# Performance work log

Measured on AMD Instinct MI355X. Metric: run time of the kernel, lower is better.

The kernel has to match this reference:

```python
import jax, jax.numpy as jnp
import numpy as np
import math

# init config (matches init_kwargs); sigma/alpha are squared in __init__
SIGMA2 = 8.0 ** 2
ALPHA2 = 8.0 ** 2
C_SIZE = 512
STRIDE = 8
MINX = 1e-06
M = 100                      # ratio=100 > 1 -> M = int(ratio), capped at 100
K = C_SIZE // STRIDE         # 64 grid cells per axis
G = K * K                    # 4096 density-field cells
B, N = 8, 512                # images, annotated points per image
TWO_PI = 2.0 * math.pi


def setup_inputs():
    key = jax.random.key(0)
    k1, _ = jax.random.split(key)
    points = jax.random.uniform(k1, (B, N, 2), dtype=jnp.float32) * C_SIZE
    st_sizes = jnp.full((B,), float(C_SIZE), dtype=jnp.float32)
    return {"points": points, "st_sizes": st_sizes}


def _per_image(pts, cood):
    # pts: [N,2]; cood: [K]
    x = pts[:, 0]
    y = pts[:, 1]
    dx = x[:, None] - cood[None, :]                 # [N,K]
    dy = y[:, None] - cood[None, :]                 # [N,K]
    # dis_all = y_dis[:, :, None] + x_dis[:, None, :] flattened: g = iy*K + ix
    dis = (dy[:, :, None] ** 2 + dx[:, None, :] ** 2).reshape(pts.shape[0], G)  # [N,G]
    s1 = ALPHA2 + SIGMA2
    s2 = ALPHA2 + SIGMA2 / 2.0
    m = jnp.exp(-0.5 / s1 * dis) / (TWO_PI * s1)    # [N,G]
    tv = jnp.exp(-0.5 / s2 * dis) / (TWO_PI * s2)
    v = (tv / (TWO_PI * 2.0 * SIGMA2)).sum(0) - (m ** 2).sum(0)   # [G] (sel_v == v, no bg)
    # top-M cells by sel_v, then sort indices ascending (ratio>1 branch -> static M)
    inds = jnp.argsort(-v)
    Minds = jnp.sort(inds[:M])                      # [M]
    v = jnp.maximum(v, MINX)                        # add=False -> clamp
    # xf[n, iy*K+ix] = x_n - cood[ix]; yf[n, iy*K+ix] = y_n - cood[iy]
    iy = Minds // K
    ix = Minds % K
    xfM = dx[:, ix]                                 # [N,M]
    yfM = dy[:, iy]                                 # [N,M]
    df = (xfM[:, None, :] - xfM[:, :, None]) ** 2 + (yfM[:, None, :] - yfM[:, :, None]) ** 2
    af = (0.5 * (xfM[:, None, :] + xfM[:, :, None])) ** 2 + (0.5 * (yfM[:, None, :] + yfM[:, :, None])) ** 2
    g1 = jnp.exp(-0.5 / (2.0 * SIGMA2) * df) / (TWO_PI * 2.0 * SIGMA2)          # [N,M,M]
    tmpv2 = (g1 * (jnp.exp(-0.5 / s2 * af) / (TWO_PI * s2))).sum(0) + g1.sum(0)  # [M,M]
    disM = dis[:, Minds]                            # [N,M]
    tmpm2 = jnp.exp(-0.5 / s1 * disM) / (TWO_PI * s1)
    A = tmpv2 - tmpm2.T @ tmpm2                     # [M,M]
    eye = jnp.eye(M, dtype=bool)
    A = jnp.where(eye, 1e-10, A)                    # diag overwritten to 1e-10
    vM = v[Minds] + 1e-10
    tmpA = vM[:, None] * jnp.linalg.inv(A) * vM[None, :] + jnp.diag(vM)
    Bm = jnp.linalg.inv(tmpA)
    return m, v, A, Bm, Minds


def reference(points, st_sizes):
    # st_sizes only matters for use_background=True; kept for signature fidelity
    cood = jnp.arange(0, C_SIZE, STRIDE, dtype=jnp.float32) + STRIDE / 2.0
    m, v, A, Bm, Minds = jax.vmap(lambda p: _per_image(p, cood))(points)
    return m, v, A, Bm, Minds
```

## Files before the change

kernel.cpp:

```cpp
#include <hip/hip_runtime.h>
#include <math.h>

#ifndef M_PI
#define M_PI 3.14159265358979323846
#endif

#define BB 8
#define NN 512
#define KK 64
#define GG 4096
#define MM 100

#define SZ_VD    (BB*GG*8u*2u)
#define OFF_VD   0u
#define SZ_VM    (BB*MM*4u)
#define OFF_VM   (OFF_VD + SZ_VD)
#define SZ_AD    (BB*MM*MM*4u)
#define OFF_AD   (OFF_VM + SZ_VM)

#define OUT_M  0
#define OUT_V  (BB*NN*GG)
#define OUT_A  (OUT_V + BB*GG)
#define OUT_B  (OUT_A + BB*MM*MM)
#define OUT_MI (OUT_B + BB*MM*MM)

#define MU_PER 8
#define MU_VP 4096
#define MU_AS 2048
#define MU_IV 10240

__device__ __forceinline__ void m_units(const float* __restrict__ pts,
                                        float* __restrict__ out, int u0, int cnt) {
  const float CM = (float)(1.0/(2.0*M_PI*128.0));
  for (int k = 0; k < cnt; ++k) {
    int u = u0 + k;
    int t = u*256 + (int)threadIdx.x;
    int e = t << 2;
    int img = e >> 21;
    int rem = e & ((1 << 21) - 1);
    int n = rem >> 12;
    int g = rem & 4095;
    int iy = g >> 6, ix = g & 63;
    float x = pts[(img*NN + n)*2 + 0];
    float y = pts[(img*NN + n)*2 + 1];
    float dy = y - (8.0f*iy + 4.0f);
    float ey = __expf(dy*dy*(-0.5f/128.0f));
    float4 r;
    float dx0 = x - (8.0f*ix + 4.0f);
    float dx1 = x - (8.0f*(ix+1) + 4.0f);
    float dx2 = x - (8.0f*(ix+2) + 4.0f);
    float dx3 = x - (8.0f*(ix+3) + 4.0f);
    r.x = ey*__expf(dx0*dx0*(-0.5f/128.0f))*CM;
    r.y = ey*__expf(dx1*dx1*(-0.5f/128.0f))*CM;
    r.z = ey*__expf(dx2*dx2*(-0.5f/128.0f))*CM;
    r.w = ey*__expf(dx3*dx3*(-0.5f/128.0f))*CM;
    *reinterpret_cast<float4*>(&out[OUT_M + e]) = r;
  }
}

__device__ __forceinline__ void m_units512(const float* __restrict__ pts,
                                           float* __restrict__ out, int u0, int cnt) {
  const float CM = (float)(1.0/(2.0*M_PI*128.0));
  for (int k = 0; k < cnt/2; ++k) {
    int t = u0*256 + k*512 + (int)threadIdx.x;
    int e = t << 2;
    int img = e >> 21;
    int rem = e & ((1 << 21) - 1);
    int n = rem >> 12;
    int g = rem & 4095;
    int iy = g >> 6, ix = g & 63;
    float x = pts[(img*NN + n)*2 + 0];
    float y = pts[(img*NN + n)*2 + 1];
    float dy = y - (8.0f*iy + 4.0f);
    float ey = __expf(dy*dy*(-0.5f/128.0f));
    float4 r;
    float dx0 = x - (8.0f*ix + 4.0f);
    float dx1 = x - (8.0f*(ix+1) + 4.0f);
    float dx2 = x - (8.0f*(ix+2) + 4.0f);
    float dx3 = x - (8.0f*(ix+3) + 4.0f);
    r.x = ey*__expf(dx0*dx0*(-0.5f/128.0f))*CM;
    r.y = ey*__expf(dx1*dx1*(-0.5f/128.0f))*CM;
    r.z = ey*__expf(dx2*dx2*(-0.5f/128.0f))*CM;
    r.w = ey*__expf(dx3*dx3*(-0.5f/128.0f))*CM;
    *reinterpret_cast<float4*>(&out[OUT_M + e]) = r;
  }
}

__device__ __forceinline__ float flt_readlane(float v, int l) {
  return __int_as_float(__builtin_amdgcn_readlane(__float_as_int(v), l));
}

__global__ __launch_bounds__(256) void k_vpart(const float* __restrict__ pts,
                                               double* __restrict__ vd,
                                               float* __restrict__ out) {
  __shared__ double sEy2[16][66], sEy3[16][66], sEx2[16][66], sEx3[16][66];
  __shared__ float px[256], py[256];
  int bid = blockIdx.x;
  if (bid >= BB*32) { m_units(pts, out, (bid - BB*32)*MU_PER, MU_PER); return; }
  int half = bid & 1;
  int rem = bid >> 1;
  int tile = rem & 15;
  int img = rem >> 4;
  int iy0 = (tile >> 2) << 4;
  int ix0 = (tile & 3) << 4;
  int tx = threadIdx.x & 15, ty = threadIdx.x >> 4;
  int n = threadIdx.x & 63;
  int tbl = threadIdx.x >> 6;
  for (int s = threadIdx.x; s < 256; s += 256) {
    px[s] = pts[(img*NN + half*256 + s)*2 + 0];
    py[s] = pts[(img*NN + half*256 + s)*2 + 1];
  }
  const double alpha = (tbl & 1) ? (1.0/128.0) : (0.5/96.0);
  const double Q = exp(-128.0*alpha);
  const int base = (tbl >= 2) ? ix0 : iy0;
  double* dst = (tbl == 0) ? &sEy2[0][0] : (tbl == 1) ? &sEy3[0][0]
              : (tbl == 2) ? &sEx2[0][0] : &sEx3[0][0];
  double aV = 0.0, aM = 0.0;
  for (int kc = 0; kc < 4; ++kc) {
    int nbl = kc << 6;
    __syncthreads();
    {
      int nn = nbl + n;
      double coord = (tbl >= 2) ? (double)px[nn] : (double)py[nn];
      double d0 = coord - (8.0*base + 4.0);
      double E = exp(-alpha*d0*d0);
      double R = exp(alpha*(16.0*d0 - 64.0));
      #pragma unroll
      for (int row = 0; row < 16; ++row) {
        dst[row*66 + n] = E;
        E *= R; R *= Q;
      }
    }
    __syncthreads();
    #pragma unroll 8
    for (int n2 = 0; n2 < 64; ++n2) {
      aV += sEy2[ty][n2]*sEx2[tx][n2];
      aM += sEy3[ty][n2]*sEx3[tx][n2];
    }
  }
  const double CTV = 1.0/((2.0*M_PI*96.0)*(2.0*M_PI*128.0));
  const double CM2 = 1.0/((2.0*M_PI*128.0)*(2.0*M_PI*128.0));
  vd[half*(BB*GG) + img*GG + (iy0 + ty)*KK + ix0 + tx] = CTV*aV - CM2*aM;
}

union AselU {
  struct {
    unsigned int ku[GG];
    unsigned int hist4[4][256];
    unsigned int wq[4];
    unsigned int sPref, sMask;
    unsigned int sRem, sPickB, sPickRem, sCGt, sCEq;
    int tie[128];
  } se;
  struct {
    float sxi[16][130], syi[16][130], sti[16][130];
    float sxj[16][130], syj[16][130], stj[16][130];
    float px[NN], py[NN];
    float cxi[16], cyi[16], cxj[16], cyj[16];
  } ka;
};

__device__ __forceinline__ void bitonic128(int* a, int tid) {
  for (int kk = 2; kk <= 128; kk <<= 1)
    for (int jj = kk >> 1; jj > 0; jj >>= 1) {
      if (tid < 128) {
        int p = tid ^ jj;
        if (p > tid) {
          int x = a[tid], y = a[p];
          bool up = ((tid & kk) == 0);
          if (up ? (x > y) : (x < y)) { a[tid] = y; a[p] = x; }
        }
      }
      __syncthreads();
    }
}

__global__ __launch_bounds__(256) void k_Asel(const float* __restrict__ pts,
                                              const double* __restrict__ vd,
                                              float* __restrict__ out,
                                              float* __restrict__ ad,
                                              float* __restrict__ vm) {
  __shared__ AselU u;
  __shared__ int selFinal[128];
  int bid = blockIdx.x;
  if (bid >= BB*28) { m_units(pts, out, MU_VP + (bid - BB*28)*MU_PER, MU_PER); return; }
  int img = bid / 28;
  int tile = bid - img*28;
  bool tile0 = (tile == 0);
  int tid = threadIdx.x;
  int wv = tid >> 6;
  int lane = tid & 63;

  for (int t = 0; t < 16; ++t) {
    int g = t*256 + tid;
    float v = (float)(vd[img*GG + g] + vd[BB*GG + img*GG + g]);
    if (tile0) out[OUT_V + img*GG + g] = fmaxf(v, 1e-6f);
    int w = __float_as_int(v);
    u.se.ku[g] = (w < 0) ? ~(unsigned)w : ((unsigned)w | 0x80000000u);
  }
  if (tid == 0) {
    u.se.sRem = 100; u.se.sPref = 0u; u.se.sMask = 0u;
    u.se.sCGt = 0; u.se.sCEq = 0;
  }
  for (int shift = 24; shift >= 0; shift -= 8) {
    for (int c = 0; c < 4; ++c) u.se.hist4[c][tid] = 0;
    __syncthreads();
    unsigned mask = u.se.sMask, pref = u.se.sPref;
    for (int t = 0; t < 16; ++t) {
      unsigned k = u.se.ku[t*256 + tid];
      if ((k & mask) == pref)
        atomicAdd(&u.se.hist4[wv][(k >> shift) & 255u], 1u);
    }
    __syncthreads();
    unsigned tot = u.se.hist4[0][tid] + u.se.hist4[1][tid]
                 + u.se.hist4[2][tid] + u.se.hist4[3][tid];
    unsigned val = tot;
    #pragma unroll
    for (int off = 1; off < 64; off <<= 1) {
      unsigned o = (unsigned)__shfl_down((int)val, off);
      if (lane + off < 64) val += o;
    }
    if (lane == 0) u.se.wq[wv] = val;
    __syncthreads();
    unsigned suf = val;
    for (int w2 = wv + 1; w2 < 4; ++w2) suf += u.se.wq[w2];
    unsigned rem = u.se.sRem;
    unsigned sgt = suf - tot;
    if (suf >= rem && sgt < rem) { u.se.sPickB = (unsigned)tid; u.se.sPickRem = rem - sgt; }
    __syncthreads();
    if (tid == 0) {
      u.se.sPref |= u.se.sPickB << shift;
      u.se.sMask |= 255u << shift;
      u.se.sRem   = u.se.sPickRem;
    }
    __syncthreads();
  }
  unsigned T = u.se.sPref;
  for (int t = 0; t < 16; ++t) {
    int g = t*256 + tid;
    unsigned k = u.se.ku[g];
    if (k > T) {
      unsigned p = atomicAdd(&u.se.sCGt, 1u);
      selFinal[p] = g;
    } else if (k == T) {
      unsigned p = atomicAdd(&u.se.sCEq, 1u);
      if (p < 128) u.se.tie[p] = g;
    }
  }
  __syncthreads();
  unsigned cgt = u.se.sCGt, ceq = u.se.sCEq, r = u.se.sRem;
  if (tid < 128 && tid >= (int)((ceq < 128u) ? ceq : 128u)) u.se.tie[tid] = 0x7fffffff;
  __syncthreads();
  bitonic128(u.se.tie, tid);
  if (tid < (int)r) selFinal[cgt + tid] = u.se.tie[tid];
  if (tid >= MM && tid < 128) selFinal[tid] = 0x7fffffff;
  __syncthreads();
  bitonic128(selFinal, tid);
  if (tile0 && tid < MM) {
    int mi = selFinal[tid];
    out[OUT_MI + img*MM + tid] = (float)mi;
    float vsel = (float)(vd[img*GG + mi] + vd[BB*GG + img*GG + mi]);
    vm[img*MM + tid] = fmaxf(vsel, 1e-6f) + 1e-10f;
  }
  __syncthreads();

  int it = 0, trem = tile;
  while (trem >= 7 - it) { trem -= 7 - it; ++it; }
  int jt = it + trem;
  int i0 = it*16, j0 = jt*16;
  int tj = tid & 15, ti = tid >> 4;
  int i = i0 + ti, j = j0 + tj;
  const float CM = (float)(1.0/(2.0*M_PI*128.0));
  const float C1 = (float)(1.0/(2.0*M_PI*128.0));
  const float C2 = (float)(1.0/(2.0*M_PI*96.0));
  for (int s = tid; s < NN; s += 256) {
    u.ka.px[s] = pts[(img*NN + s)*2 + 0];
    u.ka.py[s] = pts[(img*NN + s)*2 + 1];
  }
  if (tid < 16) {
    int gi = i0 + tid; if (gi > 99) gi = 99;
    int mi = selFinal[gi];
    u.ka.cxi[tid] = 8.0f*(mi & 63) + 4.0f;
    u.ka.cyi[tid] = 8.0f*(mi >> 6) + 4.0f;
  } else if (tid < 32) {
    int rr = tid - 16;
    int gj = j0 + rr; if (gj > 99) gj = 99;
    int mj = selFinal[gj];
    u.ka.cxj[rr] = 8.0f*(mj & 63) + 4.0f;
    u.ka.cyj[rr] = 8.0f*(mj >> 6) + 4.0f;
  }
  float aV = 0.0f, aM = 0.0f;
  for (int nc = 0; nc < NN; nc += 128) {
    __syncthreads();
    for (int s = tid; s < 16*128; s += 256) {
      int row = s >> 7, n = s & 127;
      float x = u.ka.px[nc + n], y = u.ka.py[nc + n];
      float fxi = x - u.ka.cxi[row], fyi = y - u.ka.cyi[row];
      u.ka.sxi[row][n] = fxi; u.ka.syi[row][n] = fyi;
      u.ka.sti[row][n] = __expf((fxi*fxi + fyi*fyi)*(-0.5f/128.0f))*CM;
      float fxj = x - u.ka.cxj[row], fyj = y - u.ka.cyj[row];
      u.ka.sxj[row][n] = fxj; u.ka.syj[row][n] = fyj;
      u.ka.stj[row][n] = __expf((fxj*fxj + fyj*fyj)*(-0.5f/128.0f))*CM;
    }
    __syncthreads();
    #pragma unroll 4
    for (int n = 0; n < 128; ++n) {
      float xi = u.ka.sxi[ti][n], yi = u.ka.syi[ti][n], tii = u.ka.sti[ti][n];
      float xj = u.ka.sxj[tj][n], yj = u.ka.syj[tj][n], tjj = u.ka.stj[tj][n];
      float ddx = xj - xi, ddy = yj - yi;
      float df = ddx*ddx + ddy*ddy;
      float sx = 0.5f*(xi + xj), sy = 0.5f*(yi + yj);
      float af = sx*sx + sy*sy;
      float g1 = __expf(df*(-0.5f/128.0f))*C1;
      float h  = __expf(af*(-0.5f/96.0f))*C2;
      aV += g1 + g1*h;
      aM += tii*tjj;
    }
  }
  if (i < 100 && j < 100) {
    float val = (i == j) ? 1e-10f : (float)((double)aV - (double)aM);
    out[OUT_A + (img*MM + i)*MM + j] = val;
    ad[(img*MM + i)*MM + j] = val;
    if (it != jt) {
      out[OUT_A + (img*MM + j)*MM + i] = val;
      ad[(img*MM + j)*MM + i] = val;
    }
  }
}

#define PRS 130
__global__ __launch_bounds__(512)
void k_inv_m(const float* __restrict__ ad,
             const float* __restrict__ vm,
             const float* __restrict__ pts,
             float* __restrict__ out) {
  __shared__ float S[128*17];
  __shared__ float Pr[16*PRS];
  __shared__ float svm[112];
  if (blockIdx.x >= BB) {
    m_units512(pts, out, MU_VP + MU_AS + ((int)blockIdx.x - BB)*MU_PER, MU_PER);
    return;
  }
  int img = blockIdx.x;
  int tx = threadIdx.x & 31, ty = threadIdx.x >> 5;
  float C[7][4];
  if (threadIdx.x < 100) svm[threadIdx.x] = vm[img*MM + threadIdx.x];
  #pragma unroll
  for (int a = 0; a < 7; ++a) {
    int r = ty + 16*a;
    #pragma unroll
    for (int b = 0; b < 4; ++b) {
      int col = tx + 32*b;
      float v2 = (r < 100 && col < 100) ? ad[(img*MM + r)*MM + col] : 0.0f;
      if (r == col && r < 100) v2 += vm[img*MM + r];
      C[a][b] = v2;
    }
  }
  for (int p = 0; p < 7; ++p) {
    int k0 = p*16;
    int nbp = (p == 6) ? 4 : 16;
    {
      int bp = p >> 1;
      bool mine = ((tx >> 4) == (p & 1));
      int cq = tx & 15;
      #pragma unroll
      for (int a = 0; a < 7; ++a) {
        int r = ty + 16*a;
        if (mine) {
          float val = 0.0f;
          #pragma unroll
          for (int b = 0; b < 4; ++b) if (b == bp) val = C[a][b];
          S[r*17 + cq] = (r < 100 && cq < nbp) ? val : 0.0f;
        }
      }
    }
    {
      float pv[4];
      #pragma unroll
      for (int b = 0; b < 4; ++b) pv[b] = 0.0f;
      #pragma unroll
      for (int a = 0; a < 7; ++a) {
        #pragma unroll
        for (int b = 0; b < 4; ++b) if (a == p) pv[b] = C[a][b];
      }
      #pragma unroll
      for (int b = 0; b < 4; ++b) Pr[ty*PRS + tx + 32*b] = pv[b];
    }
    __syncthreads();
    if (threadIdx.x < 64) {
      int lane = threadIdx.x;
      float P0[16], P1[16];
      #pragma unroll
      for (int c = 0; c < 16; ++c) {
        P0[c] = S[lane*17 + c];
        P1[c] = (lane + 64 < 112) ? S[(lane + 64)*17 + c] : 0.0f;
      }
      #pragma unroll
      for (int kk = 0; kk < 16; ++kk) {
        if (kk < nbp) {
          int kg = k0 + kk;
          int r1 = lane + 64;
          bool khigh = kg >= 64; int kl = kg & 63;
          float pivinv = 1.0f / flt_readlane(khigh ? P1[kk] : P0[kk], kl);
          float pr[16];
          #pragma unroll
          for (int c = 0; c < 16; ++c) {
            float pv = flt_readlane(khigh ? P1[c] : P0[c], kl);
            pr[c] = (c == kk) ? pivinv : pv*pivinv;
          }
          {
            float f = P0[kk];
            if (lane == kg) {
              #pragma unroll
              for (int c = 0; c < 16; ++c) P0[c] = pr[c];
            } else {
              #pragma unroll
              for (int c = 0; c < 16; ++c) P0[c] = ((c == kk) ? 0.0f : P0[c]) - f*pr[c];
            }
          }
          {
            float f = P1[kk];
            if (r1 == kg) {
              #pragma unroll
              for (int c = 0; c < 16; ++c) P1[c] = pr[c];
            } else {
              #pragma unroll
              for (int c = 0; c < 16; ++c) P1[c] = ((c == kk) ? 0.0f : P1[c]) - f*pr[c];
            }
          }
        }
      }
      #pragma unroll
      for (int c = 0; c < 16; ++c) {
        S[lane*17 + c] = P0[c];
        if (lane + 64 < 112) S[(lane + 64)*17 + c] = P1[c];
      }
    }
    __syncthreads();
    #pragma unroll
    for (int a = 0; a < 7; ++a) {
      int r = ty + 16*a;
      bool prow_ = (r >= k0) && (r < k0 + 16);
      #pragma unroll
      for (int b = 0; b < 4; ++b) {
        int col = tx + 32*b;
        if (r >= 100 || (col >> 4) == p || prow_) C[a][b] = 0.0f;
      }
    }
    #pragma unroll 4
    for (int t = 0; t < 16; ++t) {
      bool tok = (t < nbp);
      float bt[4], sa[7];
      #pragma unroll
      for (int b = 0; b < 4; ++b) bt[b] = tok ? Pr[t*PRS + tx + 32*b] : 0.0f;
      #pragma unroll
      for (int a = 0; a < 7; ++a) sa[a] = S[(ty + 16*a)*17 + t];
      #pragma unroll
      for (int a = 0; a < 7; ++a)
        #pragma unroll
        for (int b = 0; b < 4; ++b) C[a][b] += sa[a]*bt[b];
    }
    #pragma unroll
    for (int a = 0; a < 7; ++a) {
      int r = ty + 16*a;
      #pragma unroll
      for (int b = 0; b < 4; ++b) {
        int col = tx + 32*b;
        if ((col >> 4) == p) C[a][b] = S[r*17 + (col & 15)];
      }
    }
    __syncthreads();
  }
  #pragma unroll
  for (int a = 0; a < 7; ++a) {
    int r = ty + 16*a; if (r >= 100) continue;
    float dinv = 1.0f / svm[r];
    #pragma unroll
    for (int b = 0; b < 4; ++b) {
      int col = tx + 32*b; if (col >= 100) continue;
      float val = ((col == r) ? dinv : 0.0f) - C[a][b];
      out[OUT_B + (img*MM + r)*MM + col] = val;
    }
  }
}

extern "C" void kernel_launch(void* const* d_in, const int* in_sizes, int n_in,
                              void* d_out, int out_size, void* d_ws, size_t ws_size,
                              hipStream_t stream) {
  const float* pts = (const float*)d_in[0];
  float* out = (float*)d_out;
  char* ws = (char*)d_ws;
  double* vd  = (double*)(ws + OFF_VD);
  float* vmd = (float*)(ws + OFF_VM);
  float* ad  = (float*)(ws + OFF_AD);

  hipLaunchKernelGGL(k_vpart, dim3(BB*32 + MU_VP/MU_PER), dim3(256), 0, stream, pts, vd, out);
  hipLaunchKernelGGL(k_Asel, dim3(BB*28 + MU_AS/MU_PER), dim3(256), 0, stream, pts, vd, out, ad, vmd);
  hipLaunchKernelGGL(k_inv_m, dim3(BB + MU_IV/MU_PER), dim3(512), 0, stream, ad, vmd, pts, out);
}
```

Baseline: 195.8 us.

## Split v partial sums four ways, spread histogram atomics, wave-level bitonic sort

The v-field reduction kernel now splits the 512 points into four quarters instead of two, doubling the number of blocks, and reads LDS as double2 pairs. The top-M radix select spreads its histogram over 32 padded copies to reduce LDS atomic contention. The two block-wide bitonic sorts with many __syncthreads become a single-wave register sort using shuffles. In exchange, the workspace grows, k_Asel must read four partial buffers, and clearing and summing the histograms costs more.

```diff
diff --git a/kernel.cpp b/kernel.cpp
--- a/kernel.cpp
+++ b/kernel.cpp
@@ -11,7 +11,7 @@
 #define GG 4096
 #define MM 100
 
-#define SZ_VD    (BB*GG*8u*2u)
+#define SZ_VD    (BB*GG*8u*4u)
 #define OFF_VD   0u
 #define SZ_VM    (BB*MM*4u)
 #define OFF_VM   (OFF_VD + SZ_VD)
@@ -94,11 +94,11 @@
                                                double* __restrict__ vd,
                                                float* __restrict__ out) {
   __shared__ double sEy2[16][66], sEy3[16][66], sEx2[16][66], sEx3[16][66];
-  __shared__ float px[256], py[256];
+  __shared__ float px[128], py[128];
   int bid = blockIdx.x;
-  if (bid >= BB*32) { m_units(pts, out, (bid - BB*32)*MU_PER, MU_PER); return; }
-  int half = bid & 1;
-  int rem = bid >> 1;
+  if (bid >= BB*64) { m_units(pts, out, (bid - BB*64)*MU_PER, MU_PER); return; }
+  int quarter = bid & 3;
+  int rem = bid >> 2;
   int tile = rem & 15;
   int img = rem >> 4;
   int iy0 = (tile >> 2) << 4;
@@ -106,9 +106,9 @@
   int tx = threadIdx.x & 15, ty = threadIdx.x >> 4;
   int n = threadIdx.x & 63;
   int tbl = threadIdx.x >> 6;
-  for (int s = threadIdx.x; s < 256; s += 256) {
-    px[s] = pts[(img*NN + half*256 + s)*2 + 0];
-    py[s] = pts[(img*NN + half*256 + s)*2 + 1];
+  if (threadIdx.x < 128) {
+    px[threadIdx.x] = pts[(img*NN + quarter*128 + threadIdx.x)*2 + 0];
+    py[threadIdx.x] = pts[(img*NN + quarter*128 + threadIdx.x)*2 + 1];
   }
   const double alpha = (tbl & 1) ? (1.0/128.0) : (0.5/96.0);
   const double Q = exp(-128.0*alpha);
@@ -116,7 +116,7 @@
   double* dst = (tbl == 0) ? &sEy2[0][0] : (tbl == 1) ? &sEy3[0][0]
               : (tbl == 2) ? &sEx2[0][0] : &sEx3[0][0];
   double aV = 0.0, aM = 0.0;
-  for (int kc = 0; kc < 4; ++kc) {
+  for (int kc = 0; kc < 2; ++kc) {
     int nbl = kc << 6;
     __syncthreads();
     {
@@ -133,20 +133,24 @@
     }
     __syncthreads();
     #pragma unroll 8
-    for (int n2 = 0; n2 < 64; ++n2) {
-      aV += sEy2[ty][n2]*sEx2[tx][n2];
-      aM += sEy3[ty][n2]*sEx3[tx][n2];
+    for (int n2 = 0; n2 < 64; n2 += 2) {
+      double2 y2 = *reinterpret_cast<const double2*>(&sEy2[ty][n2]);
+      double2 x2 = *reinterpret_cast<const double2*>(&sEx2[tx][n2]);
+      double2 y3 = *reinterpret_cast<const double2*>(&sEy3[ty][n2]);
+      double2 x3 = *reinterpret_cast<const double2*>(&sEx3[tx][n2]);
+      aV += y2.x*x2.x; aV += y2.y*x2.y;
+      aM += y3.x*x3.x; aM += y3.y*x3.y;
     }
   }
   const double CTV = 1.0/((2.0*M_PI*96.0)*(2.0*M_PI*128.0));
   const double CM2 = 1.0/((2.0*M_PI*128.0)*(2.0*M_PI*128.0));
-  vd[half*(BB*GG) + img*GG + (iy0 + ty)*KK + ix0 + tx] = CTV*aV - CM2*aM;
+  vd[quarter*(BB*GG) + img*GG + (iy0 + ty)*KK + ix0 + tx] = CTV*aV - CM2*aM;
 }
 
 union AselU {
   struct {
     unsigned int ku[GG];
-    unsigned int hist4[4][256];
+    unsigned int hist[32][257];
     unsigned int wq[4];
     unsigned int sPref, sMask;
     unsigned int sRem, sPickB, sPickRem, sCGt, sCEq;
@@ -160,19 +164,24 @@
   } ka;
 };
 
-__device__ __forceinline__ void bitonic128(int* a, int tid) {
-  for (int kk = 2; kk <= 128; kk <<= 1)
-    for (int jj = kk >> 1; jj > 0; jj >>= 1) {
-      if (tid < 128) {
-        int p = tid ^ jj;
-        if (p > tid) {
-          int x = a[tid], y = a[p];
-          bool up = ((tid & kk) == 0);
-          if (up ? (x > y) : (x < y)) { a[tid] = y; a[p] = x; }
-        }
-      }
-      __syncthreads();
-    }
+__device__ __forceinline__ void wave_sort128(int* a) {
+  int L = (int)(threadIdx.x & 63);
+  int e0 = a[2*L], e1 = a[2*L + 1];
+  for (int kk = 2; kk <= 128; kk <<= 1) {
+    for (int jj = kk >> 1; jj >= 2; jj >>= 1) {
+      int pl = jj >> 1;
+      int o0 = __shfl_xor(e0, pl);
+      int o1 = __shfl_xor(e1, pl);
+      bool upper = (L & pl) != 0;
+      bool up = ((2*L) & kk) == 0;
+      if (up != upper) { e0 = min(e0, o0); e1 = min(e1, o1); }
+      else             { e0 = max(e0, o0); e1 = max(e1, o1); }
+    }
+    bool up = ((2*L) & kk) == 0;
+    int lo = min(e0, e1), hi = max(e0, e1);
+    e0 = up ? lo : hi; e1 = up ? hi : lo;
+  }
+  a[2*L] = e0; a[2*L + 1] = e1;
 }
 
 __global__ __launch_bounds__(256) void k_Asel(const float* __restrict__ pts,
@@ -190,10 +199,12 @@
   int tid = threadIdx.x;
   int wv = tid >> 6;
   int lane = tid & 63;
+  int hc = tid >> 3;
 
   for (int t = 0; t < 16; ++t) {
     int g = t*256 + tid;
-    float v = (float)(vd[img*GG + g] + vd[BB*GG + img*GG + g]);
+    float v = (float)(((vd[img*GG + g] + vd[BB*GG + img*GG + g])
+                     + vd[2*BB*GG + img*GG + g]) + vd[3*BB*GG + img*GG + g]);
     if (tile0) out[OUT_V + img*GG + g] = fmaxf(v, 1e-6f);
     int w = __float_as_int(v);
     u.se.ku[g] = (w < 0) ? ~(unsigned)w : ((unsigned)w | 0x80000000u);
@@ -203,17 +214,18 @@
     u.se.sCGt = 0; u.se.sCEq = 0;
   }
   for (int shift = 24; shift >= 0; shift -= 8) {
-    for (int c = 0; c < 4; ++c) u.se.hist4[c][tid] = 0;
+    for (int s = tid; s < 32*257; s += 256) (&u.se.hist[0][0])[s] = 0;
     __syncthreads();
     unsigned mask = u.se.sMask, pref = u.se.sPref;
     for (int t = 0; t < 16; ++t) {
       unsigned k = u.se.ku[t*256 + tid];
       if ((k & mask) == pref)
-        atomicAdd(&u.se.hist4[wv][(k >> shift) & 255u], 1u);
-    }
-    __syncthreads();
-    unsigned tot = u.se.hist4[0][tid] + u.se.hist4[1][tid]
-                 + u.se.hist4[2][tid] + u.se.hist4[3][tid];
+        atomicAdd(&u.se.hist[hc][(k >> shift) & 255u], 1u);
+    }
+    __syncthreads();
+    unsigned tot = 0;
+    #pragma unroll
+    for (int c = 0; c < 32; ++c) tot += u.se.hist[c][tid];
     unsigned val = tot;
     #pragma unroll
     for (int off = 1; off < 64; off <<= 1) {
@@ -251,15 +263,18 @@
   unsigned cgt = u.se.sCGt, ceq = u.se.sCEq, r = u.se.sRem;
   if (tid < 128 && tid >= (int)((ceq < 128u) ? ceq : 128u)) u.se.tie[tid] = 0x7fffffff;
   __syncthreads();
-  bitonic128(u.se.tie, tid);
+  if (tid < 64) wave_sort128(u.se.tie);
+  __syncthreads();
   if (tid < (int)r) selFinal[cgt + tid] = u.se.tie[tid];
   if (tid >= MM && tid < 128) selFinal[tid] = 0x7fffffff;
   __syncthreads();
-  bitonic128(selFinal, tid);
+  if (tid < 64) wave_sort128(selFinal);
+  __syncthreads();
   if (tile0 && tid < MM) {
     int mi = selFinal[tid];
     out[OUT_MI + img*MM + tid] = (float)mi;
-    float vsel = (float)(vd[img*GG + mi] + vd[BB*GG + img*GG + mi]);
+    float vsel = (float)(((vd[img*GG + mi] + vd[BB*GG + img*GG + mi])
+                        + vd[2*BB*GG + img*GG + mi]) + vd[3*BB*GG + img*GG + mi]);
     vm[img*MM + tid] = fmaxf(vsel, 1e-6f) + 1e-10f;
   }
   __syncthreads();
@@ -494,7 +509,7 @@
   float* vmd = (float*)(ws + OFF_VM);
   float* ad  = (float*)(ws + OFF_AD);
 
-  hipLaunchKernelGGL(k_vpart, dim3(BB*32 + MU_VP/MU_PER), dim3(256), 0, stream, pts, vd, out);
+  hipLaunchKernelGGL(k_vpart, dim3(BB*64 + MU_VP/MU_PER), dim3(256), 0, stream, pts, vd, out);
   hipLaunchKernelGGL(k_Asel, dim3(BB*28 + MU_AS/MU_PER), dim3(256), 0, stream, pts, vd, out, ad, vmd);
   hipLaunchKernelGGL(k_inv_m, dim3(BB + MU_IV/MU_PER), dim3(512), 0, stream, ad, vmd, pts, out);
 }
```

Result: no change. 193.8 us (-1.0%).
